# Optimization experiments

Measured on AMD Instinct MI355X. Metric: run time of the kernel, lower is better.

The kernel has to match this reference:

```python
import jax, jax.numpy as jnp
import numpy as np

BSZ, ILEN, TLEN = 64, 1024, 1024
IDIM, HDIM, NCLASSES = 128, 256, 128


def setup_inputs() -> dict:
    key = jax.random.key(0)
    ks = jax.random.split(key, 5)
    # xavier-ish scaling for weights
    w_ih = jax.random.normal(ks[0], (4 * HDIM, IDIM), jnp.float32) * (2.0 / (4 * HDIM + IDIM)) ** 0.5
    w_hh = jax.random.normal(ks[1], (4 * HDIM, HDIM), jnp.float32) * (2.0 / (4 * HDIM + HDIM)) ** 0.5
    b = jnp.zeros((4 * HDIM,), jnp.float32)
    clf_w = jax.random.normal(ks[2], (NCLASSES, HDIM), jnp.float32) * (2.0 / (NCLASSES + HDIM)) ** 0.5
    clf_b = jnp.zeros((NCLASSES,), jnp.float32)
    inp = jax.random.normal(ks[3], (BSZ, ILEN, IDIM), jnp.float32)
    return {"inp": inp, "tlen": TLEN, "w_ih": w_ih, "w_hh": w_hh, "b": b,
            "clf_w": clf_w, "clf_b": clf_b}


def reference(inp, tlen, w_ih, w_hh, b, clf_w, clf_b):
    bsz, ilen, _ = inp.shape
    hdim = w_hh.shape[1]
    # pad tlen zero timesteps at the end (F.pad [0,0,0,tlen])
    inp_padded = jnp.pad(inp, ((0, 0), (0, tlen), (0, 0)))  # [B, ilen+tlen, idim]
    xs = jnp.swapaxes(inp_padded, 0, 1)  # [T, B, idim]

    def step(carry, x_t):
        h, c = carry
        z = x_t @ w_ih.T + h @ w_hh.T + b  # [B, 4H]
        i, f, g, o = jnp.split(z, 4, axis=-1)
        i = jax.nn.sigmoid(i)
        f = jax.nn.sigmoid(f)
        g = jnp.tanh(g)
        o = jax.nn.sigmoid(o)
        c_new = f * c + i * g
        h_new = o * jnp.tanh(c_new)
        return (h_new, c_new), h_new

    h0 = jnp.zeros((bsz, hdim), inp.dtype)
    c0 = jnp.zeros((bsz, hdim), inp.dtype)
    _, hs = jax.lax.scan(step, (h0, c0), xs)  # [T, B, H]
    hs = jnp.swapaxes(hs, 0, 1)  # [B, T, H]
    probs = hs @ clf_w.T + clf_b  # [B, T, nclasses]
    return probs[:, ilen:]
```

## Files before the change

kernel.cpp:

```cpp
#include <hip/hip_runtime.h>
#include <hip/hip_fp16.h>

#define BSZ   64
#define ILEN  1024
#define TLEN  1024
#define TTOT  2048
#define IDIM  128
#define HDIM  256
#define GDIM  1024
#define NCLS  128
#define NGRP  8
#define NMEM  4
#define BPG   8

typedef unsigned int u32;
typedef _Float16 f16x8 __attribute__((ext_vector_type(8)));
typedef float f32x4 __attribute__((ext_vector_type(4)));
typedef _Float16 h2_t __attribute__((ext_vector_type(2)));

union U4H8 { uint4 u; f16x8 h; };

__device__ __forceinline__ float fdot2(u32 a, u32 b, float acc) {
#if __has_builtin(__builtin_amdgcn_fdot2)
    union { u32 u; h2_t h; } ua, ub;
    ua.u = a; ub.u = b;
    return __builtin_amdgcn_fdot2(ua.h, ub.h, acc, false);
#else
    union { u32 u; __half2 h; } ua, ub;
    ua.u = a; ub.u = b;
    return acc + __low2float(ua.h) * __low2float(ub.h)
               + __high2float(ua.h) * __high2float(ub.h);
#endif
}

__device__ __forceinline__ u32 packf2(float x, float y) {
    __half2 h = __floats2half2_rn(x, y);
    union { __half2 h; u32 u; } c; c.h = h;
    return c.u;
}

__device__ __forceinline__ float sigm(float x) { return 1.f / (1.f + __expf(-x)); }
__device__ __forceinline__ float tanh_fast(float x) { return 1.f - 2.f / (__expf(2.f * x) + 1.f); }

__global__ void pack_kernel(const float* __restrict__ w_ih,
                            const float* __restrict__ w_hh,
                            const float* __restrict__ clf_w,
                            uint4* __restrict__ Apack,
                            uint4* __restrict__ Aipack,
                            uint4* __restrict__ Wcq)
{
    int i = blockIdx.x * blockDim.x + threadIdx.x;
    if (i < 32768) {
        int ci = i >> 6, l = i & 63;
        int ug = ci >> 5, g = (ci >> 3) & 3, kt = ci & 7;
        int R  = g * HDIM + ug * 16 + (l & 15);
        int K0 = kt * 32 + (l >> 4) * 8;
        const float* src = w_hh + (size_t)R * HDIM + K0;
        uint4 v;
        v.x = packf2(src[0], src[1]); v.y = packf2(src[2], src[3]);
        v.z = packf2(src[4], src[5]); v.w = packf2(src[6], src[7]);
        Apack[i] = v;
    } else if (i < 49152) {
        int r = i - 32768;
        int ci = r >> 6, l = r & 63;
        int ug = ci >> 4, g = (ci >> 2) & 3, kt4 = ci & 3;
        int R  = g * HDIM + ug * 16 + (l & 15);
        int K0 = kt4 * 32 + (l >> 4) * 8;
        const float* src = w_ih + (size_t)R * IDIM + K0;
        uint4 v;
        v.x = packf2(src[0], src[1]); v.y = packf2(src[2], src[3]);
        v.z = packf2(src[4], src[5]); v.w = packf2(src[6], src[7]);
        Aipack[r] = v;
    } else if (i < 53248) {
        int r = i - 49152;
        int n = r & (NCLS - 1);
        int k4 = r >> 7;
        const float* src = clf_w + (size_t)n * HDIM + k4 * 8;
        uint4 v;
        v.x = packf2(src[0], src[1]); v.y = packf2(src[2], src[3]);
        v.z = packf2(src[4], src[5]); v.w = packf2(src[6], src[7]);
        Wcq[r] = v;
    }
}

__global__ void init_kernel(u32* __restrict__ hbuf, u32* __restrict__ flags)
{
    int i = blockIdx.x * blockDim.x + threadIdx.x;
    if (i < NGRP * 2 * BPG * 128) hbuf[i] = 0u;
    if (i < NGRP * 16) flags[i] = 0u;
}

__global__ __launch_bounds__(256, 1) void lstm_rec(
    const float* __restrict__ inp,
    const float* __restrict__ bias_g,
    const uint4* __restrict__ Apack,
    const uint4* __restrict__ Aipack,
    __half* __restrict__ Hs,
    u32* __restrict__ hbuf,
    u32* __restrict__ flags)
{
    __shared__ alignas(16) uint4 whA[128 * 64];
    __shared__ alignas(16) u32   hB[16 * 132];
    __shared__ float z_sh[4 * BPG * 72];

    const int blk    = blockIdx.x;
    const int g      = blk & 7;
    const int member = blk >> 3;
    const int tid = threadIdx.x;
    const int w   = tid >> 6;
    const int l   = tid & 63;
    const int lq  = l >> 4;
    const int lm  = l & 15;

    #pragma unroll
    for (int s = 0; s < 32; ++s) {
        int gi = s * 256 + tid;
        int d  = gi >> 6, l2 = gi & 63;
        int gate = d >> 5, rt = (d >> 3) & 3, kt = d & 7;
        whA[gi] = Apack[(((member * 4 + rt) * 32) + gate * 8 + kt) * 64 + l2];
    }

    float bias_r[4][4];
    #pragma unroll
    for (int rt = 0; rt < 4; ++rt)
        #pragma unroll
        for (int r = 0; r < 4; ++r)
            bias_r[rt][r] = bias_g[w * HDIM + member * 64 + rt * 16 + lq * 4 + r];

    const int b_e = tid >> 5;
    const int u2  = tid & 31;
    float c0 = 0.f, c1 = 0.f;

    const uint4* hB4 = (const uint4*)hB;
    u32* fl = flags + g * 16;

    for (int t = 0; t < TTOT; ++t) {
        uint4 bx[4];
        uint4 wiAr[4][4];
        if (t < ILEN) {
            if (lm < 8) {
                const float* xr = inp + ((size_t)(g * 8 + lm) * ILEN + t) * IDIM + lq * 8;
                #pragma unroll
                for (int kt4 = 0; kt4 < 4; ++kt4) {
                    float4 a = *(const float4*)(xr + kt4 * 32);
                    float4 b = *(const float4*)(xr + kt4 * 32 + 4);
                    bx[kt4].x = packf2(a.x, a.y);
                    bx[kt4].y = packf2(a.z, a.w);
                    bx[kt4].z = packf2(b.x, b.y);
                    bx[kt4].w = packf2(b.z, b.w);
                }
            }
            #pragma unroll
            for (int rt = 0; rt < 4; ++rt)
                #pragma unroll
                for (int kt4 = 0; kt4 < 4; ++kt4)
                    wiAr[rt][kt4] = Aipack[(((member * 4 + rt) * 16) + w * 4 + kt4) * 64 + l];
        }

        if (t > 0) {
            while (true) {
                u32 v = __hip_atomic_load(fl + (l & 3), __ATOMIC_ACQUIRE,
                                          __HIP_MEMORY_SCOPE_AGENT);
                if (__all(v >= (u32)t)) break;
                __builtin_amdgcn_s_sleep(1);
            }
        }

        {
            const int r  = tid >> 5;
            const int c0i = (tid & 31) * 4;
            const u32* hr = hbuf + (((size_t)g * 2 + (t & 1)) * BPG + r) * 128 + c0i;
            u32 v0 = __hip_atomic_load(hr + 0, __ATOMIC_RELAXED, __HIP_MEMORY_SCOPE_AGENT);
            u32 v1 = __hip_atomic_load(hr + 1, __ATOMIC_RELAXED, __HIP_MEMORY_SCOPE_AGENT);
            u32 v2 = __hip_atomic_load(hr + 2, __ATOMIC_RELAXED, __HIP_MEMORY_SCOPE_AGENT);
            u32 v3 = __hip_atomic_load(hr + 3, __ATOMIC_RELAXED, __HIP_MEMORY_SCOPE_AGENT);
            hB[r * 132 + c0i + 0] = v0;
            hB[r * 132 + c0i + 1] = v1;
            hB[r * 132 + c0i + 2] = v2;
            hB[r * 132 + c0i + 3] = v3;
        }

        f32x4 acc[4];
        #pragma unroll
        for (int rt = 0; rt < 4; ++rt)
            acc[rt] = (f32x4){bias_r[rt][0], bias_r[rt][1], bias_r[rt][2], bias_r[rt][3]};
        if (t < ILEN) {
            #pragma unroll
            for (int kt4 = 0; kt4 < 4; ++kt4) {
                U4H8 b; b.u = bx[kt4];
                #pragma unroll
                for (int rt = 0; rt < 4; ++rt) {
                    U4H8 a; a.u = wiAr[rt][kt4];
                    acc[rt] = __builtin_amdgcn_mfma_f32_16x16x32_f16(a.h, b.h, acc[rt], 0, 0, 0);
                }
            }
        }
        __syncthreads();

        #pragma unroll
        for (int kt = 0; kt < 8; ++kt) {
            U4H8 b; b.u = hB4[lm * 33 + kt * 4 + lq];
            #pragma unroll
            for (int rt = 0; rt < 4; ++rt) {
                U4H8 a; a.u = whA[((w * 4 + rt) * 8 + kt) * 64 + l];
                acc[rt] = __builtin_amdgcn_mfma_f32_16x16x32_f16(a.h, b.h, acc[rt], 0, 0, 0);
            }
        }

        if (lm < 8) {
            #pragma unroll
            for (int rt = 0; rt < 4; ++rt)
                #pragma unroll
                for (int r = 0; r < 4; ++r)
                    z_sh[(w * BPG + lm) * 72 + rt * 16 + lq * 4 + r] = acc[rt][r];
        }
        __syncthreads();

        {
            float zi0 = z_sh[(0 * BPG + b_e) * 72 + 2 * u2];
            float zi1 = z_sh[(0 * BPG + b_e) * 72 + 2 * u2 + 1];
            float zf0 = z_sh[(1 * BPG + b_e) * 72 + 2 * u2];
            float zf1 = z_sh[(1 * BPG + b_e) * 72 + 2 * u2 + 1];
            float zg0 = z_sh[(2 * BPG + b_e) * 72 + 2 * u2];
            float zg1 = z_sh[(2 * BPG + b_e) * 72 + 2 * u2 + 1];
            float zo0 = z_sh[(3 * BPG + b_e) * 72 + 2 * u2];
            float zo1 = z_sh[(3 * BPG + b_e) * 72 + 2 * u2 + 1];
            c0 = sigm(zf0) * c0 + sigm(zi0) * tanh_fast(zg0);
            c1 = sigm(zf1) * c1 + sigm(zi1) * tanh_fast(zg1);
            float h0 = sigm(zo0) * tanh_fast(c0);
            float h1 = sigm(zo1) * tanh_fast(c1);
            u32 hp = packf2(h0, h1);
            __hip_atomic_store(hbuf + (((size_t)g * 2 + ((t + 1) & 1)) * BPG + b_e) * 128
                                    + member * 32 + u2,
                               hp, __ATOMIC_RELAXED, __HIP_MEMORY_SCOPE_AGENT);
            if (t >= ILEN) {
                u32* hsrow = (u32*)(Hs + ((size_t)(g * 8 + b_e) * TLEN + (t - ILEN)) * HDIM
                                       + member * 64);
                hsrow[u2] = hp;
            }
        }
        __syncthreads();

        if (tid == 0)
            __hip_atomic_store(&fl[member], (u32)(t + 1), __ATOMIC_RELEASE,
                               __HIP_MEMORY_SCOPE_AGENT);
    }
}

#define CTT 16
__global__ __launch_bounds__(256) void clf_kernel(
    const uint4* __restrict__ Wcq,
    const __half* __restrict__ Hs,
    const float* __restrict__ clf_b,
    float* __restrict__ out)
{
    __shared__ alignas(16) u32 h_sh[CTT * (HDIM / 2)];
    const int tid = threadIdx.x;
    const int b  = blockIdx.x >> 6;
    const int t0 = (blockIdx.x & 63) * CTT;

    const uint4* hsrc = (const uint4*)(Hs + ((size_t)b * TLEN + t0) * HDIM);
    uint4* hdst = (uint4*)h_sh;
    hdst[tid]       = hsrc[tid];
    hdst[tid + 256] = hsrc[tid + 256];
    __syncthreads();

    const int n  = tid & (NCLS - 1);
    const int tl = tid >> 7;
    const float bias = clf_b[n];
    float acc[8];
    #pragma unroll
    for (int q = 0; q < 8; ++q) acc[q] = bias;

    #pragma unroll 4
    for (int k4 = 0; k4 < HDIM / 8; ++k4) {
        uint4 w = Wcq[k4 * NCLS + n];
        #pragma unroll
        for (int q = 0; q < 8; ++q) {
            const uint4* hp = (const uint4*)(h_sh + (tl + 2 * q) * (HDIM / 2));
            uint4 h = hp[k4];
            acc[q] = fdot2(w.x, h.x, acc[q]);
            acc[q] = fdot2(w.y, h.y, acc[q]);
            acc[q] = fdot2(w.z, h.z, acc[q]);
            acc[q] = fdot2(w.w, h.w, acc[q]);
        }
    }
    #pragma unroll
    for (int q = 0; q < 8; ++q) {
        out[((size_t)b * TLEN + t0 + tl + 2 * q) * NCLS + n] = acc[q];
    }
}

extern "C" void kernel_launch(void* const* d_in, const int* in_sizes, int n_in,
                              void* d_out, int out_size, void* d_ws, size_t ws_size,
                              hipStream_t stream)
{
    const float* inp   = (const float*)d_in[0];
    const float* w_ih  = (const float*)d_in[2];
    const float* w_hh  = (const float*)d_in[3];
    const float* bias  = (const float*)d_in[4];
    const float* clf_w = (const float*)d_in[5];
    const float* clf_b = (const float*)d_in[6];
    float* out = (float*)d_out;

    char* ws = (char*)d_ws;
    uint4*  Apack  = (uint4*)(ws);
    uint4*  Aipack = (uint4*)(ws + 524288);
    uint4*  Wcq    = (uint4*)(ws + 786432);
    __half* Hs     = (__half*)(ws + 851968);
    u32*    hbuf   = (u32*)(ws + 34406400);
    u32*    flags  = (u32*)(ws + 34471936);

    init_kernel<<<64, 256, 0, stream>>>(hbuf, flags);
    pack_kernel<<<208, 256, 0, stream>>>(w_ih, w_hh, clf_w, Apack, Aipack, Wcq);

    void* args[] = {(void*)&inp, (void*)&bias, (void*)&Apack, (void*)&Aipack,
                    (void*)&Hs, (void*)&hbuf, (void*)&flags};
    hipLaunchCooperativeKernel((const void*)lstm_rec,
                               dim3(NGRP * NMEM), dim3(256), args, 0, stream);

    clf_kernel<<<BSZ * (TLEN / CTT), 256, 0, stream>>>(Wcq, Hs, clf_b, out);
}
```

Measured before the change: 7.689 ms.

## Restructure LSTM recurrence into 8 blocks each handling two 16-batch groups

Regroups the batch into 4 groups of 16 rows (filling the MFMA 16-column tile instead of 8), and each of 8 blocks processes two groups interleaved so one group's gate math overlaps the other's wait. Hidden state is read directly from global into registers rather than staged through LDS, the z_sh shared-memory transpose and block barriers are removed, and each wave computes gate nonlinearities from its own accumulators while signalling per-wave flags. This cuts synchronisation and LDS traffic per timestep but uses far fewer CUs, streams the input-weight fragments from global every step, and relies on the packed weight layout matching the new indexing.

```diff
diff --git a/kernel.cpp b/kernel.cpp
--- a/kernel.cpp
+++ b/kernel.cpp
@@ -9,9 +9,9 @@
 #define HDIM  256
 #define GDIM  1024
 #define NCLS  128
-#define NGRP  8
+#define NGRP  4
 #define NMEM  4
-#define BPG   8
+#define BPG   16
 
 typedef unsigned int u32;
 typedef _Float16 f16x8 __attribute__((ext_vector_type(8)));
@@ -100,150 +100,156 @@
     u32* __restrict__ flags)
 {
     __shared__ alignas(16) uint4 whA[128 * 64];
-    __shared__ alignas(16) u32   hB[16 * 132];
-    __shared__ float z_sh[4 * BPG * 72];
 
     const int blk    = blockIdx.x;
-    const int g      = blk & 7;
-    const int member = blk >> 3;
+    const int member = blk & 3;
+    const int q      = blk >> 2;
+    const int gA     = q * 2 + 0;
+    const int gB     = q * 2 + 1;
     const int tid = threadIdx.x;
     const int w   = tid >> 6;
     const int l   = tid & 63;
     const int lq  = l >> 4;
     const int lm  = l & 15;
 
+    {
+        const uint4* src = Apack + (size_t)member * 8192;
+        #pragma unroll
+        for (int s = 0; s < 32; ++s) whA[s * 256 + tid] = src[s * 256 + tid];
+    }
+    __syncthreads();
+
+    f32x4 biasv[4];
     #pragma unroll
-    for (int s = 0; s < 32; ++s) {
-        int gi = s * 256 + tid;
-        int d  = gi >> 6, l2 = gi & 63;
-        int gate = d >> 5, rt = (d >> 3) & 3, kt = d & 7;
-        whA[gi] = Apack[(((member * 4 + rt) * 32) + gate * 8 + kt) * 64 + l2];
-    }
-
-    float bias_r[4][4];
-    #pragma unroll
-    for (int rt = 0; rt < 4; ++rt)
-        #pragma unroll
-        for (int r = 0; r < 4; ++r)
-            bias_r[rt][r] = bias_g[w * HDIM + member * 64 + rt * 16 + lq * 4 + r];
-
-    const int b_e = tid >> 5;
-    const int u2  = tid & 31;
-    float c0 = 0.f, c1 = 0.f;
-
-    const uint4* hB4 = (const uint4*)hB;
-    u32* fl = flags + g * 16;
+    for (int g = 0; g < 4; ++g) {
+        const float* bp = bias_g + g * HDIM + member * 64 + w * 16 + lq * 4;
+        biasv[g] = (f32x4){bp[0], bp[1], bp[2], bp[3]};
+    }
+
+    float cA[4] = {0.f, 0.f, 0.f, 0.f};
+    float cB[4] = {0.f, 0.f, 0.f, 0.f};
+
+    const uint4* hb4 = (const uint4*)hbuf;
+    u32* flA = flags + gA * 16;
+    u32* flB = flags + gB * 16;
+    const int fidx = l & 15;
+    const int fA = gA * 16 + member * 4 + w;
+    const int fB = gB * 16 + member * 4 + w;
 
     for (int t = 0; t < TTOT; ++t) {
-        uint4 bx[4];
-        uint4 wiAr[4][4];
+        const int par  = t & 1;
+        const int par2 = (t + 1) & 1;
+
+        uint4 bxA[4], bxB[4];
         if (t < ILEN) {
-            if (lm < 8) {
-                const float* xr = inp + ((size_t)(g * 8 + lm) * ILEN + t) * IDIM + lq * 8;
-                #pragma unroll
-                for (int kt4 = 0; kt4 < 4; ++kt4) {
-                    float4 a = *(const float4*)(xr + kt4 * 32);
-                    float4 b = *(const float4*)(xr + kt4 * 32 + 4);
-                    bx[kt4].x = packf2(a.x, a.y);
-                    bx[kt4].y = packf2(a.z, a.w);
-                    bx[kt4].z = packf2(b.x, b.y);
-                    bx[kt4].w = packf2(b.z, b.w);
-                }
-            }
-            #pragma unroll
-            for (int rt = 0; rt < 4; ++rt)
-                #pragma unroll
-                for (int kt4 = 0; kt4 < 4; ++kt4)
-                    wiAr[rt][kt4] = Aipack[(((member * 4 + rt) * 16) + w * 4 + kt4) * 64 + l];
+            const float* xA = inp + ((size_t)(gA * 16 + lm) * ILEN + t) * IDIM + lq * 8;
+            const float* xB = inp + ((size_t)(gB * 16 + lm) * ILEN + t) * IDIM + lq * 8;
+            #pragma unroll
+            for (int k4 = 0; k4 < 4; ++k4) {
+                float4 a0 = *(const float4*)(xA + k4 * 32);
+                float4 a1 = *(const float4*)(xA + k4 * 32 + 4);
+                bxA[k4].x = packf2(a0.x, a0.y); bxA[k4].y = packf2(a0.z, a0.w);
+                bxA[k4].z = packf2(a1.x, a1.y); bxA[k4].w = packf2(a1.z, a1.w);
+                float4 b0 = *(const float4*)(xB + k4 * 32);
+                float4 b1 = *(const float4*)(xB + k4 * 32 + 4);
+                bxB[k4].x = packf2(b0.x, b0.y); bxB[k4].y = packf2(b0.z, b0.w);
+                bxB[k4].z = packf2(b1.x, b1.y); bxB[k4].w = packf2(b1.z, b1.w);
+            }
         }
 
         if (t > 0) {
             while (true) {
-                u32 v = __hip_atomic_load(fl + (l & 3), __ATOMIC_ACQUIRE,
-                                          __HIP_MEMORY_SCOPE_AGENT);
+                u32 v = __hip_atomic_load(flA + fidx, __ATOMIC_ACQUIRE, __HIP_MEMORY_SCOPE_AGENT);
                 if (__all(v >= (u32)t)) break;
                 __builtin_amdgcn_s_sleep(1);
             }
-        }
-
+            while (true) {
+                u32 v = __hip_atomic_load(flB + fidx, __ATOMIC_ACQUIRE, __HIP_MEMORY_SCOPE_AGENT);
+                if (__all(v >= (u32)t)) break;
+                __builtin_amdgcn_s_sleep(1);
+            }
+        }
+
+        uint4 hA[8], hB[8];
         {
-            const int r  = tid >> 5;
-            const int c0i = (tid & 31) * 4;
-            const u32* hr = hbuf + (((size_t)g * 2 + (t & 1)) * BPG + r) * 128 + c0i;
-            u32 v0 = __hip_atomic_load(hr + 0, __ATOMIC_RELAXED, __HIP_MEMORY_SCOPE_AGENT);
-            u32 v1 = __hip_atomic_load(hr + 1, __ATOMIC_RELAXED, __HIP_MEMORY_SCOPE_AGENT);
-            u32 v2 = __hip_atomic_load(hr + 2, __ATOMIC_RELAXED, __HIP_MEMORY_SCOPE_AGENT);
-            u32 v3 = __hip_atomic_load(hr + 3, __ATOMIC_RELAXED, __HIP_MEMORY_SCOPE_AGENT);
-            hB[r * 132 + c0i + 0] = v0;
-            hB[r * 132 + c0i + 1] = v1;
-            hB[r * 132 + c0i + 2] = v2;
-            hB[r * 132 + c0i + 3] = v3;
-        }
-
-        f32x4 acc[4];
+            const uint4* pA = hb4 + ((size_t)(gA * 2 + par) * BPG + lm) * 32 + lq;
+            const uint4* pB = hb4 + ((size_t)(gB * 2 + par) * BPG + lm) * 32 + lq;
+            #pragma unroll
+            for (int kt = 0; kt < 8; ++kt) { hA[kt] = pA[kt * 4]; hB[kt] = pB[kt * 4]; }
+        }
+
+        f32x4 accA[4], accB[4];
         #pragma unroll
-        for (int rt = 0; rt < 4; ++rt)
-            acc[rt] = (f32x4){bias_r[rt][0], bias_r[rt][1], bias_r[rt][2], bias_r[rt][3]};
+        for (int g = 0; g < 4; ++g) { accA[g] = biasv[g]; accB[g] = biasv[g]; }
         if (t < ILEN) {
             #pragma unroll
-            for (int kt4 = 0; kt4 < 4; ++kt4) {
-                U4H8 b; b.u = bx[kt4];
+            for (int k4 = 0; k4 < 4; ++k4) {
+                U4H8 bA, bB; bA.u = bxA[k4]; bB.u = bxB[k4];
                 #pragma unroll
-                for (int rt = 0; rt < 4; ++rt) {
-                    U4H8 a; a.u = wiAr[rt][kt4];
-                    acc[rt] = __builtin_amdgcn_mfma_f32_16x16x32_f16(a.h, b.h, acc[rt], 0, 0, 0);
+                for (int g = 0; g < 4; ++g) {
+                    U4H8 a; a.u = Aipack[((size_t)(member * 4 + w) * 16 + g * 4 + k4) * 64 + l];
+                    accA[g] = __builtin_amdgcn_mfma_f32_16x16x32_f16(a.h, bA.h, accA[g], 0, 0, 0);
+                    accB[g] = __builtin_amdgcn_mfma_f32_16x16x32_f16(a.h, bB.h, accB[g], 0, 0, 0);
                 }
             }
         }
-        __syncthreads();
-
         #pragma unroll
         for (int kt = 0; kt < 8; ++kt) {
-            U4H8 b; b.u = hB4[lm * 33 + kt * 4 + lq];
-            #pragma unroll
-            for (int rt = 0; rt < 4; ++rt) {
-                U4H8 a; a.u = whA[((w * 4 + rt) * 8 + kt) * 64 + l];
-                acc[rt] = __builtin_amdgcn_mfma_f32_16x16x32_f16(a.h, b.h, acc[rt], 0, 0, 0);
-            }
-        }
-
-        if (lm < 8) {
-            #pragma unroll
-            for (int rt = 0; rt < 4; ++rt)
-                #pragma unroll
-                for (int r = 0; r < 4; ++r)
-                    z_sh[(w * BPG + lm) * 72 + rt * 16 + lq * 4 + r] = acc[rt][r];
-        }
-        __syncthreads();
+            U4H8 bA, bB; bA.u = hA[kt]; bB.u = hB[kt];
+            #pragma unroll
+            for (int g = 0; g < 4; ++g) {
+                U4H8 a; a.u = whA[((w * 4 + g) * 8 + kt) * 64 + l];
+                accA[g] = __builtin_amdgcn_mfma_f32_16x16x32_f16(a.h, bA.h, accA[g], 0, 0, 0);
+                accB[g] = __builtin_amdgcn_mfma_f32_16x16x32_f16(a.h, bB.h, accB[g], 0, 0, 0);
+            }
+        }
 
         {
-            float zi0 = z_sh[(0 * BPG + b_e) * 72 + 2 * u2];
-            float zi1 = z_sh[(0 * BPG + b_e) * 72 + 2 * u2 + 1];
-            float zf0 = z_sh[(1 * BPG + b_e) * 72 + 2 * u2];
-            float zf1 = z_sh[(1 * BPG + b_e) * 72 + 2 * u2 + 1];
-            float zg0 = z_sh[(2 * BPG + b_e) * 72 + 2 * u2];
-            float zg1 = z_sh[(2 * BPG + b_e) * 72 + 2 * u2 + 1];
-            float zo0 = z_sh[(3 * BPG + b_e) * 72 + 2 * u2];
-            float zo1 = z_sh[(3 * BPG + b_e) * 72 + 2 * u2 + 1];
-            c0 = sigm(zf0) * c0 + sigm(zi0) * tanh_fast(zg0);
-            c1 = sigm(zf1) * c1 + sigm(zi1) * tanh_fast(zg1);
-            float h0 = sigm(zo0) * tanh_fast(c0);
-            float h1 = sigm(zo1) * tanh_fast(c1);
-            u32 hp = packf2(h0, h1);
-            __hip_atomic_store(hbuf + (((size_t)g * 2 + ((t + 1) & 1)) * BPG + b_e) * 128
-                                    + member * 32 + u2,
-                               hp, __ATOMIC_RELAXED, __HIP_MEMORY_SCOPE_AGENT);
+            float hv[4];
+            #pragma unroll
+            for (int r = 0; r < 4; ++r) {
+                float ig = sigm(accA[0][r]);
+                float fg = sigm(accA[1][r]);
+                float gg = tanh_fast(accA[2][r]);
+                float og = sigm(accA[3][r]);
+                cA[r] = fg * cA[r] + ig * gg;
+                hv[r] = og * tanh_fast(cA[r]);
+            }
+            uint2 pv; pv.x = packf2(hv[0], hv[1]); pv.y = packf2(hv[2], hv[3]);
+            u32* dst = hbuf + ((size_t)(gA * 2 + par2) * BPG + lm) * 128
+                            + member * 32 + w * 8 + lq * 2;
+            *(uint2*)dst = pv;
             if (t >= ILEN) {
-                u32* hsrow = (u32*)(Hs + ((size_t)(g * 8 + b_e) * TLEN + (t - ILEN)) * HDIM
-                                       + member * 64);
-                hsrow[u2] = hp;
-            }
-        }
-        __syncthreads();
-
-        if (tid == 0)
-            __hip_atomic_store(&fl[member], (u32)(t + 1), __ATOMIC_RELEASE,
-                               __HIP_MEMORY_SCOPE_AGENT);
+                u32* hs = (u32*)(Hs + ((size_t)(gA * 16 + lm) * TLEN + (t - ILEN)) * HDIM)
+                          + member * 32 + w * 8 + lq * 2;
+                *(uint2*)hs = pv;
+            }
+        }
+        if (l == 0)
+            __hip_atomic_store(&flags[fA], (u32)(t + 1), __ATOMIC_RELEASE, __HIP_MEMORY_SCOPE_AGENT);
+        {
+            float hv[4];
+            #pragma unroll
+            for (int r = 0; r < 4; ++r) {
+                float ig = sigm(accB[0][r]);
+                float fg = sigm(accB[1][r]);
+                float gg = tanh_fast(accB[2][r]);
+                float og = sigm(accB[3][r]);
+                cB[r] = fg * cB[r] + ig * gg;
+                hv[r] = og * tanh_fast(cB[r]);
+            }
+            uint2 pv; pv.x = packf2(hv[0], hv[1]); pv.y = packf2(hv[2], hv[3]);
+            u32* dst = hbuf + ((size_t)(gB * 2 + par2) * BPG + lm) * 128
+                            + member * 32 + w * 8 + lq * 2;
+            *(uint2*)dst = pv;
+            if (t >= ILEN) {
+                u32* hs = (u32*)(Hs + ((size_t)(gB * 16 + lm) * TLEN + (t - ILEN)) * HDIM)
+                          + member * 32 + w * 8 + lq * 2;
+                *(uint2*)hs = pv;
+            }
+        }
+        if (l == 0)
+            __hip_atomic_store(&flags[fB], (u32)(t + 1), __ATOMIC_RELEASE, __HIP_MEMORY_SCOPE_AGENT);
     }
 }
 
@@ -317,7 +323,7 @@
     void* args[] = {(void*)&inp, (void*)&bias, (void*)&Apack, (void*)&Aipack,
                     (void*)&Hs, (void*)&hbuf, (void*)&flags};
     hipLaunchCooperativeKernel((const void*)lstm_rec,
-                               dim3(NGRP * NMEM), dim3(256), args, 0, stream);
+                               dim3(NMEM * 2), dim3(256), args, 0, stream);
 
     clf_kernel<<<BSZ * (TLEN / CTT), 256, 0, stream>>>(Wcq, Hs, clf_b, out);
 }
```

New measurement: 17.68 ms. 130% more time.

## Remove LDS staging and block barriers from LSTM recurrence with per-wave flags

Applied to the files above, without the earlier changes.

Reorganizes the recurrent step so each wave owns all four gates for its own 16 hidden units. The gate nonlinearities and cell update then run directly on MFMA accumulators, with no LDS round trip through z_sh. Hidden state is read straight from global memory into registers instead of being staged through shared memory. Each wave publishes its own flag, so all __syncthreads in the time loop go away and consumers poll 16 per-wave flags. The risks are more flag-polling traffic, redundant global loads of h by every wave, and a changed Apack/bias layout that must match the host packing.

```diff
diff --git a/kernel.cpp b/kernel.cpp
--- a/kernel.cpp
+++ b/kernel.cpp
@@ -100,8 +100,6 @@
     u32* __restrict__ flags)
 {
     __shared__ alignas(16) uint4 whA[128 * 64];
-    __shared__ alignas(16) u32   hB[16 * 132];
-    __shared__ float z_sh[4 * BPG * 72];
 
     const int blk    = blockIdx.x;
     const int g      = blk & 7;
@@ -111,139 +109,116 @@
     const int l   = tid & 63;
     const int lq  = l >> 4;
     const int lm  = l & 15;
-
+    const int bm  = lm & 7;
+
+    {
+        const uint4* src = Apack + (size_t)member * 8192;
+        #pragma unroll
+        for (int s = 0; s < 32; ++s) whA[s * 256 + tid] = src[s * 256 + tid];
+    }
+    __syncthreads();
+
+    f32x4 biasv[4];
     #pragma unroll
-    for (int s = 0; s < 32; ++s) {
-        int gi = s * 256 + tid;
-        int d  = gi >> 6, l2 = gi & 63;
-        int gate = d >> 5, rt = (d >> 3) & 3, kt = d & 7;
-        whA[gi] = Apack[(((member * 4 + rt) * 32) + gate * 8 + kt) * 64 + l2];
-    }
-
-    float bias_r[4][4];
-    #pragma unroll
-    for (int rt = 0; rt < 4; ++rt)
-        #pragma unroll
-        for (int r = 0; r < 4; ++r)
-            bias_r[rt][r] = bias_g[w * HDIM + member * 64 + rt * 16 + lq * 4 + r];
-
-    const int b_e = tid >> 5;
-    const int u2  = tid & 31;
-    float c0 = 0.f, c1 = 0.f;
-
-    const uint4* hB4 = (const uint4*)hB;
+    for (int gg = 0; gg < 4; ++gg) {
+        const float* bp = bias_g + gg * HDIM + member * 64 + w * 16 + lq * 4;
+        biasv[gg] = (f32x4){bp[0], bp[1], bp[2], bp[3]};
+    }
+
+    float cS[4] = {0.f, 0.f, 0.f, 0.f};
+
+    const uint4* hb4 = (const uint4*)hbuf;
     u32* fl = flags + g * 16;
+    const int fslot = g * 16 + member * 4 + w;
+    const int fidx  = l & 15;
 
     for (int t = 0; t < TTOT; ++t) {
+        const int par  = t & 1;
+        const int par2 = (t + 1) & 1;
+
         uint4 bx[4];
         uint4 wiAr[4][4];
         if (t < ILEN) {
-            if (lm < 8) {
-                const float* xr = inp + ((size_t)(g * 8 + lm) * ILEN + t) * IDIM + lq * 8;
+            const float* xr = inp + ((size_t)(g * 8 + bm) * ILEN + t) * IDIM + lq * 8;
+            #pragma unroll
+            for (int k4 = 0; k4 < 4; ++k4) {
+                float4 a0 = *(const float4*)(xr + k4 * 32);
+                float4 a1 = *(const float4*)(xr + k4 * 32 + 4);
+                bx[k4].x = packf2(a0.x, a0.y); bx[k4].y = packf2(a0.z, a0.w);
+                bx[k4].z = packf2(a1.x, a1.y); bx[k4].w = packf2(a1.z, a1.w);
+            }
+            #pragma unroll
+            for (int gg = 0; gg < 4; ++gg)
                 #pragma unroll
-                for (int kt4 = 0; kt4 < 4; ++kt4) {
-                    float4 a = *(const float4*)(xr + kt4 * 32);
-                    float4 b = *(const float4*)(xr + kt4 * 32 + 4);
-                    bx[kt4].x = packf2(a.x, a.y);
-                    bx[kt4].y = packf2(a.z, a.w);
-                    bx[kt4].z = packf2(b.x, b.y);
-                    bx[kt4].w = packf2(b.z, b.w);
-                }
-            }
-            #pragma unroll
-            for (int rt = 0; rt < 4; ++rt)
-                #pragma unroll
-                for (int kt4 = 0; kt4 < 4; ++kt4)
-                    wiAr[rt][kt4] = Aipack[(((member * 4 + rt) * 16) + w * 4 + kt4) * 64 + l];
+                for (int k4 = 0; k4 < 4; ++k4)
+                    wiAr[gg][k4] = Aipack[((size_t)(member * 4 + w) * 16 + gg * 4 + k4) * 64 + l];
         }
 
         if (t > 0) {
             while (true) {
-                u32 v = __hip_atomic_load(fl + (l & 3), __ATOMIC_ACQUIRE,
+                u32 v = __hip_atomic_load(fl + fidx, __ATOMIC_ACQUIRE,
                                           __HIP_MEMORY_SCOPE_AGENT);
                 if (__all(v >= (u32)t)) break;
                 __builtin_amdgcn_s_sleep(1);
             }
         }
 
+        uint4 hA[8];
         {
-            const int r  = tid >> 5;
-            const int c0i = (tid & 31) * 4;
-            const u32* hr = hbuf + (((size_t)g * 2 + (t & 1)) * BPG + r) * 128 + c0i;
-            u32 v0 = __hip_atomic_load(hr + 0, __ATOMIC_RELAXED, __HIP_MEMORY_SCOPE_AGENT);
-            u32 v1 = __hip_atomic_load(hr + 1, __ATOMIC_RELAXED, __HIP_MEMORY_SCOPE_AGENT);
-            u32 v2 = __hip_atomic_load(hr + 2, __ATOMIC_RELAXED, __HIP_MEMORY_SCOPE_AGENT);
-            u32 v3 = __hip_atomic_load(hr + 3, __ATOMIC_RELAXED, __HIP_MEMORY_SCOPE_AGENT);
-            hB[r * 132 + c0i + 0] = v0;
-            hB[r * 132 + c0i + 1] = v1;
-            hB[r * 132 + c0i + 2] = v2;
-            hB[r * 132 + c0i + 3] = v3;
+            const uint4* pA = hb4 + ((size_t)(g * 2 + par) * BPG + bm) * 32 + lq;
+            #pragma unroll
+            for (int kt = 0; kt < 8; ++kt) hA[kt] = pA[kt * 4];
         }
 
         f32x4 acc[4];
         #pragma unroll
-        for (int rt = 0; rt < 4; ++rt)
-            acc[rt] = (f32x4){bias_r[rt][0], bias_r[rt][1], bias_r[rt][2], bias_r[rt][3]};
+        for (int gg = 0; gg < 4; ++gg) acc[gg] = biasv[gg];
         if (t < ILEN) {
             #pragma unroll
-            for (int kt4 = 0; kt4 < 4; ++kt4) {
-                U4H8 b; b.u = bx[kt4];
+            for (int k4 = 0; k4 < 4; ++k4) {
+                U4H8 b; b.u = bx[k4];
                 #pragma unroll
-                for (int rt = 0; rt < 4; ++rt) {
-                    U4H8 a; a.u = wiAr[rt][kt4];
-                    acc[rt] = __builtin_amdgcn_mfma_f32_16x16x32_f16(a.h, b.h, acc[rt], 0, 0, 0);
+                for (int gg = 0; gg < 4; ++gg) {
+                    U4H8 a; a.u = wiAr[gg][k4];
+                    acc[gg] = __builtin_amdgcn_mfma_f32_16x16x32_f16(a.h, b.h, acc[gg], 0, 0, 0);
                 }
             }
         }
-        __syncthreads();
-
         #pragma unroll
         for (int kt = 0; kt < 8; ++kt) {
-            U4H8 b; b.u = hB4[lm * 33 + kt * 4 + lq];
-            #pragma unroll
-            for (int rt = 0; rt < 4; ++rt) {
-                U4H8 a; a.u = whA[((w * 4 + rt) * 8 + kt) * 64 + l];
-                acc[rt] = __builtin_amdgcn_mfma_f32_16x16x32_f16(a.h, b.h, acc[rt], 0, 0, 0);
-            }
-        }
-
+            U4H8 b; b.u = hA[kt];
+            #pragma unroll
+            for (int gg = 0; gg < 4; ++gg) {
+                U4H8 a; a.u = whA[((w * 4 + gg) * 8 + kt) * 64 + l];
+                acc[gg] = __builtin_amdgcn_mfma_f32_16x16x32_f16(a.h, b.h, acc[gg], 0, 0, 0);
+            }
+        }
+
+        uint2 pv;
         if (lm < 8) {
-            #pragma unroll
-            for (int rt = 0; rt < 4; ++rt)
-                #pragma unroll
-                for (int r = 0; r < 4; ++r)
-                    z_sh[(w * BPG + lm) * 72 + rt * 16 + lq * 4 + r] = acc[rt][r];
-        }
-        __syncthreads();
-
-        {
-            float zi0 = z_sh[(0 * BPG + b_e) * 72 + 2 * u2];
-            float zi1 = z_sh[(0 * BPG + b_e) * 72 + 2 * u2 + 1];
-            float zf0 = z_sh[(1 * BPG + b_e) * 72 + 2 * u2];
-            float zf1 = z_sh[(1 * BPG + b_e) * 72 + 2 * u2 + 1];
-            float zg0 = z_sh[(2 * BPG + b_e) * 72 + 2 * u2];
-            float zg1 = z_sh[(2 * BPG + b_e) * 72 + 2 * u2 + 1];
-            float zo0 = z_sh[(3 * BPG + b_e) * 72 + 2 * u2];
-            float zo1 = z_sh[(3 * BPG + b_e) * 72 + 2 * u2 + 1];
-            c0 = sigm(zf0) * c0 + sigm(zi0) * tanh_fast(zg0);
-            c1 = sigm(zf1) * c1 + sigm(zi1) * tanh_fast(zg1);
-            float h0 = sigm(zo0) * tanh_fast(c0);
-            float h1 = sigm(zo1) * tanh_fast(c1);
-            u32 hp = packf2(h0, h1);
-            __hip_atomic_store(hbuf + (((size_t)g * 2 + ((t + 1) & 1)) * BPG + b_e) * 128
-                                    + member * 32 + u2,
-                               hp, __ATOMIC_RELAXED, __HIP_MEMORY_SCOPE_AGENT);
-            if (t >= ILEN) {
-                u32* hsrow = (u32*)(Hs + ((size_t)(g * 8 + b_e) * TLEN + (t - ILEN)) * HDIM
-                                       + member * 64);
-                hsrow[u2] = hp;
-            }
-        }
-        __syncthreads();
-
-        if (tid == 0)
-            __hip_atomic_store(&fl[member], (u32)(t + 1), __ATOMIC_RELEASE,
+            float hv[4];
+            #pragma unroll
+            for (int r = 0; r < 4; ++r) {
+                float ig = sigm(acc[0][r]);
+                float fg = sigm(acc[1][r]);
+                float gg = tanh_fast(acc[2][r]);
+                float og = sigm(acc[3][r]);
+                cS[r] = fg * cS[r] + ig * gg;
+                hv[r] = og * tanh_fast(cS[r]);
+            }
+            pv.x = packf2(hv[0], hv[1]); pv.y = packf2(hv[2], hv[3]);
+            u32* dst = hbuf + ((size_t)(g * 2 + par2) * BPG + lm) * 128
+                            + member * 32 + w * 8 + lq * 2;
+            *(uint2*)dst = pv;
+        }
+        if (l == 0)
+            __hip_atomic_store(&flags[fslot], (u32)(t + 1), __ATOMIC_RELEASE,
                                __HIP_MEMORY_SCOPE_AGENT);
+        if (lm < 8 && t >= ILEN) {
+            u32* hs = (u32*)(Hs + ((size_t)(g * 8 + lm) * TLEN + (t - ILEN)) * HDIM)
+                      + member * 32 + w * 8 + lq * 2;
+            *(uint2*)hs = pv;
+        }
     }
 }
 
```

After: 13.80 ms. 79.5% more time.
